# Performance work log

Measured on AMD Instinct MI355X. Metric: run time of the kernel, lower is better.

## Reference

```python
import jax, jax.numpy as jnp
import numpy as np

N, N_EMB, HEAD, N_SEG = 8192, 256, 64, 128  # 128 molecules x 64 atoms


def setup_inputs() -> dict:
    key = jax.random.key(0)
    k0, k1, k2, k3, k4, k5 = jax.random.split(key, 6)
    X = jax.random.normal(k0, (N, N_EMB), dtype=jnp.float32)
    Z = jax.random.normal(k1, (N, 3), dtype=jnp.float32) * 3.0  # coordinates (Angstrom-ish)
    # CSR segment boundaries: 128 equal molecules of 64 atoms
    ptr = jnp.arange(N_SEG + 1, dtype=jnp.int32) * (N // N_SEG)
    scale = 1.0 / np.sqrt(N_EMB)
    Wk = jax.random.normal(k2, (HEAD, N_EMB), dtype=jnp.float32) * scale
    Wq = jax.random.normal(k3, (HEAD, N_EMB), dtype=jnp.float32) * scale
    Wv = jax.random.normal(k4, (HEAD, N_EMB), dtype=jnp.float32) * scale
    # invr0 = (rand(1) + 0.5) / cutoff, cutoff = 4.0
    invr0 = (jax.random.uniform(k5, (1,), dtype=jnp.float32) + 0.5) / 4.0
    return {"X": X, "Z": Z, "Wk": Wk, "Wq": Wq, "Wv": Wv, "invr0": invr0, "ptr": ptr}


def reference(X, Z, Wk, Wq, Wv, invr0, ptr):
    head_size = Wk.shape[0]
    n = X.shape[0]
    K = X @ Wk.T  # [N, H]
    Q = X @ Wq.T  # [N, H]
    V = X @ Wv.T  # [N, H]
    wei = (Q @ K.T) * (head_size ** -0.5)  # [N, N]
    # block-diagonal mask from segment boundaries (== torch.block_diag of ones blocks)
    seg = jnp.searchsorted(ptr[1:], jnp.arange(n, dtype=ptr.dtype), side="right")
    mask = seg[:, None] == seg[None, :]
    wei = jnp.where(mask, wei, -jnp.inf)
    wei = jax.nn.softmax(wei, axis=-1)
    # Euclidean cdist via gram trick, safe sqrt (zero grad at d2<=0, like torch.cdist)
    z2 = jnp.sum(Z * Z, axis=-1)
    d2 = jnp.maximum(z2[:, None] + z2[None, :] - 2.0 * (Z @ Z.T), 0.0)
    dist = jnp.sqrt(jnp.where(d2 > 0, d2, 1.0)) * (d2 > 0)
    wei = wei * jnp.exp(-invr0[0] * dist)
    out = wei @ V  # [N, H]
    return out
```

## Files before the change

### kernel.cpp

```cpp
#include <hip/hip_runtime.h>

#define NATOMS 8192
#define EMB    256
#define HEAD   64
#define LDT    72
#define PB     72

typedef _Float16 f16;
typedef f16   f16x8 __attribute__((ext_vector_type(8)));
typedef f16   f16x4 __attribute__((ext_vector_type(4)));
typedef float f32x4 __attribute__((ext_vector_type(4)));

__global__ __launch_bounds__(512) void fused_kernel(
    const float* __restrict__ X, const float* __restrict__ Z,
    const float* __restrict__ Wk, const float* __restrict__ Wq,
    const float* __restrict__ Wv, const float* __restrict__ invr0p,
    float* __restrict__ out)
{
  union __align__(16) SMem {
    struct {
      f16 Xs[64 * LDT];
      f16 Ws[192 * LDT];
    } a;
    struct {
      f16 Qb[32 * PB];
      f16 Kb[64 * PB];
      f16 Vt[64 * PB];
      f16 Pb[32 * PB];
      float2 part[4][32];
      float zx[64], zy[64], zz[64];
    } b;
  };
  __shared__ SMem sm;

  const int tid  = threadIdx.x;
  const int seg  = blockIdx.x >> 1;
  const int hf   = blockIdx.x & 1;
  const int base = seg * 64;

  const int wave = tid >> 6;
  const int lane = tid & 63;
  const int fr   = lane & 15;
  const int fq   = lane >> 4;
  const int lk   = fq * 8;
  const int mf0  = (wave >> 2) * 2;
  const int nf0  = (wave & 3) * 3;

  f32x4 acc[2][3];
  #pragma unroll
  for (int m = 0; m < 2; ++m)
    #pragma unroll
    for (int n = 0; n < 3; ++n) acc[m][n] = (f32x4){0.f, 0.f, 0.f, 0.f};

  for (int c = 0; c < 4; ++c) {
    const int kc = c * 64;
    #pragma unroll
    for (int i = 0; i < 2; ++i) {
      const int idx = tid + i * 512;
      const int row = idx >> 4;
      const int k4  = (idx & 15) * 4;
      const float4 v = *reinterpret_cast<const float4*>(
          X + (size_t)(base + row) * EMB + kc + k4);
      f16x4 h = {(f16)v.x, (f16)v.y, (f16)v.z, (f16)v.w};
      *reinterpret_cast<f16x4*>(&sm.a.Xs[row * LDT + k4]) = h;
    }
    #pragma unroll
    for (int i = 0; i < 6; ++i) {
      const int idx = tid + i * 512;
      const int wr  = idx >> 4;
      const int k4  = (idx & 15) * 4;
      const float* src = (wr < 64)  ? (Wq + (size_t)wr * EMB)
                       : (wr < 128) ? (Wk + (size_t)(wr - 64) * EMB)
                                    : (Wv + (size_t)(wr - 128) * EMB);
      const float4 v = *reinterpret_cast<const float4*>(src + kc + k4);
      f16x4 h = {(f16)v.x, (f16)v.y, (f16)v.z, (f16)v.w};
      *reinterpret_cast<f16x4*>(&sm.a.Ws[wr * LDT + k4]) = h;
    }
    __syncthreads();

    #pragma unroll
    for (int ks = 0; ks < 2; ++ks) {
      const int hoff = ks * 32 + lk;
      const f16x8 a0 = *reinterpret_cast<const f16x8*>(
          &sm.a.Xs[((mf0 + 0) * 16 + fr) * LDT + hoff]);
      const f16x8 a1 = *reinterpret_cast<const f16x8*>(
          &sm.a.Xs[((mf0 + 1) * 16 + fr) * LDT + hoff]);
      #pragma unroll
      for (int n = 0; n < 3; ++n) {
        const f16x8 b = *reinterpret_cast<const f16x8*>(
            &sm.a.Ws[((nf0 + n) * 16 + fr) * LDT + hoff]);
        acc[0][n] = __builtin_amdgcn_mfma_f32_16x16x32_f16(a0, b, acc[0][n], 0, 0, 0);
        acc[1][n] = __builtin_amdgcn_mfma_f32_16x16x32_f16(a1, b, acc[1][n], 0, 0, 0);
      }
    }
    __syncthreads();
  }

  #pragma unroll
  for (int m = 0; m < 2; ++m) {
    const int mf = mf0 + m;
    const int rr = mf * 16 + fq * 4;
    #pragma unroll
    for (int n = 0; n < 3; ++n) {
      const int nf  = nf0 + n;
      const int col = nf * 16 + fr;
      if (nf < 4) {
        if ((mf >> 1) == hf) {
          const int qr = rr & 31;
          #pragma unroll
          for (int j = 0; j < 4; ++j)
            sm.b.Qb[(qr + j) * PB + col] = (f16)(acc[m][n][j] * 0.125f);
        }
      } else if (nf < 8) {
        #pragma unroll
        for (int j = 0; j < 4; ++j)
          sm.b.Kb[(rr + j) * PB + (col - 64)] = (f16)acc[m][n][j];
      } else {
        f16x4 hv = {(f16)acc[m][n][0], (f16)acc[m][n][1],
                    (f16)acc[m][n][2], (f16)acc[m][n][3]};
        *reinterpret_cast<f16x4*>(&sm.b.Vt[(col - 128) * PB + rr]) = hv;
      }
    }
  }
  if (tid < 64) {
    sm.b.zx[tid] = Z[(size_t)(base + tid) * 3 + 0];
    sm.b.zy[tid] = Z[(size_t)(base + tid) * 3 + 1];
    sm.b.zz[tid] = Z[(size_t)(base + tid) * 3 + 2];
  }
  __syncthreads();

  const int kf = wave & 3;
  const int qf = wave >> 2;
  f32x4 s = (f32x4){0.f, 0.f, 0.f, 0.f};
  #pragma unroll
  for (int hs = 0; hs < 2; ++hs) {
    const int ho = hs * 32 + lk;
    const f16x8 kfrag = *reinterpret_cast<const f16x8*>(
        &sm.b.Kb[(kf * 16 + fr) * PB + ho]);
    const f16x8 qfrag = *reinterpret_cast<const f16x8*>(
        &sm.b.Qb[(qf * 16 + fr) * PB + ho]);
    s = __builtin_amdgcn_mfma_f32_16x16x32_f16(kfrag, qfrag, s, 0, 0, 0);
  }

  float m16 = fmaxf(fmaxf(s[0], s[1]), fmaxf(s[2], s[3]));
  m16 = fmaxf(m16, __shfl_xor(m16, 16));
  m16 = fmaxf(m16, __shfl_xor(m16, 32));
  float e[4]; float s16 = 0.f;
  #pragma unroll
  for (int j = 0; j < 4; ++j) { e[j] = __expf(s[j] - m16); s16 += e[j]; }
  s16 += __shfl_xor(s16, 16);
  s16 += __shfl_xor(s16, 32);
  if (fq == 0) sm.b.part[kf][qf * 16 + fr] = make_float2(m16, s16);
  __syncthreads();

  const float2 p0 = sm.b.part[0][qf * 16 + fr];
  const float2 p1 = sm.b.part[1][qf * 16 + fr];
  const float2 p2 = sm.b.part[2][qf * 16 + fr];
  const float2 p3 = sm.b.part[3][qf * 16 + fr];
  const float mg = fmaxf(fmaxf(p0.x, p1.x), fmaxf(p2.x, p3.x));
  const float sum = p0.y * __expf(p0.x - mg) + p1.y * __expf(p1.x - mg)
                  + p2.y * __expf(p2.x - mg) + p3.y * __expf(p3.x - mg);
  const float myscale = __expf(m16 - mg) / sum;

  const float invr0 = invr0p[0];
  const int   ri = hf * 32 + qf * 16 + fr;
  const float rx = sm.b.zx[ri], ry = sm.b.zy[ri], rz = sm.b.zz[ri];
  f16x4 pv;
  #pragma unroll
  for (int j = 0; j < 4; ++j) {
    const int ka = kf * 16 + fq * 4 + j;
    const float dx = rx - sm.b.zx[ka];
    const float dy = ry - sm.b.zy[ka];
    const float dz = rz - sm.b.zz[ka];
    const float dist = sqrtf(dx * dx + dy * dy + dz * dz);
    pv[j] = (f16)(e[j] * myscale * __expf(-invr0 * dist));
  }
  *reinterpret_cast<f16x4*>(
      &sm.b.Pb[(qf * 16 + fr) * PB + kf * 16 + fq * 4]) = pv;
  __syncthreads();

  const int qf2 = wave & 1;
  const int hb  = wave >> 1;
  f32x4 o = (f32x4){0.f, 0.f, 0.f, 0.f};
  #pragma unroll
  for (int ks2 = 0; ks2 < 2; ++ks2) {
    const int ko = ks2 * 32 + lk;
    const f16x8 pf = *reinterpret_cast<const f16x8*>(
        &sm.b.Pb[(qf2 * 16 + fr) * PB + ko]);
    const f16x8 vf = *reinterpret_cast<const f16x8*>(
        &sm.b.Vt[(hb * 16 + fr) * PB + ko]);
    o = __builtin_amdgcn_mfma_f32_16x16x32_f16(pf, vf, o, 0, 0, 0);
  }
  #pragma unroll
  for (int j = 0; j < 4; ++j)
    out[(size_t)(base + hf * 32 + qf2 * 16 + fq * 4 + j) * HEAD
        + hb * 16 + fr] = o[j];
}

extern "C" void kernel_launch(void* const* d_in, const int* in_sizes, int n_in,
                              void* d_out, int out_size, void* d_ws, size_t ws_size,
                              hipStream_t stream) {
  const float* X     = (const float*)d_in[0];
  const float* Z     = (const float*)d_in[1];
  const float* Wk    = (const float*)d_in[2];
  const float* Wq    = (const float*)d_in[3];
  const float* Wv    = (const float*)d_in[4];
  const float* invr0 = (const float*)d_in[5];

  fused_kernel<<<dim3(NATOMS / 32), dim3(512), 0, stream>>>(
      X, Z, Wk, Wq, Wv, invr0, (float*)d_out);
}
```

Measured before the change: 13.49 us.

## Load full X and W tiles into LDS once instead of four K-chunks

```diff
diff --git a/kernel.cpp b/kernel.cpp
--- a/kernel.cpp
+++ b/kernel.cpp
@@ -3,7 +3,7 @@
 #define NATOMS 8192
 #define EMB    256
 #define HEAD   64
-#define LDT    72
+#define WP     264
 #define PB     72
 
 typedef _Float16 f16;
@@ -19,8 +19,8 @@
 {
   union __align__(16) SMem {
     struct {
-      f16 Xs[64 * LDT];
-      f16 Ws[192 * LDT];
+      f16 Xs[64 * WP];
+      f16 Ws[192 * WP];
     } a;
     struct {
       f16 Qb[32 * PB];
@@ -42,9 +42,64 @@
   const int lane = tid & 63;
   const int fr   = lane & 15;
   const int fq   = lane >> 4;
-  const int lk   = fq * 8;
   const int mf0  = (wave >> 2) * 2;
   const int nf0  = (wave & 3) * 3;
+
+  const float ir = invr0p[0];
+  float zr0 = 0.f, zr1 = 0.f, zr2 = 0.f;
+  if (tid < 64) {
+    const float* zp = Z + (size_t)(base + tid) * 3;
+    zr0 = zp[0]; zr1 = zp[1]; zr2 = zp[2];
+  }
+
+  float4 xv[8];
+  #pragma unroll
+  for (int i = 0; i < 8; ++i) {
+    const int f = tid + i * 512;
+    const int row = f >> 6, c4 = f & 63;
+    xv[i] = *reinterpret_cast<const float4*>(
+        X + (size_t)(base + row) * EMB + c4 * 4);
+  }
+  float4 wv1[12];
+  #pragma unroll
+  for (int i = 0; i < 12; ++i) {
+    const int f = tid + i * 512;
+    const int row = f >> 6, c4 = f & 63;
+    const float* src = (row < 64) ? (Wq + (size_t)row * EMB)
+                                  : (Wk + (size_t)(row - 64) * EMB);
+    wv1[i] = *reinterpret_cast<const float4*>(src + c4 * 4);
+  }
+  #pragma unroll
+  for (int i = 0; i < 8; ++i) {
+    const int f = tid + i * 512;
+    const int row = f >> 6, c4 = f & 63;
+    f16x4 h = {(f16)xv[i].x, (f16)xv[i].y, (f16)xv[i].z, (f16)xv[i].w};
+    *reinterpret_cast<f16x4*>(&sm.a.Xs[row * WP + c4 * 4]) = h;
+  }
+  float4 wv2[12];
+  #pragma unroll
+  for (int i = 0; i < 12; ++i) {
+    const int f = tid + (12 + i) * 512;
+    const int row = f >> 6, c4 = f & 63;
+    const float* src = (row < 128) ? (Wk + (size_t)(row - 64) * EMB)
+                                   : (Wv + (size_t)(row - 128) * EMB);
+    wv2[i] = *reinterpret_cast<const float4*>(src + c4 * 4);
+  }
+  #pragma unroll
+  for (int i = 0; i < 12; ++i) {
+    const int f = tid + i * 512;
+    const int row = f >> 6, c4 = f & 63;
+    f16x4 h = {(f16)wv1[i].x, (f16)wv1[i].y, (f16)wv1[i].z, (f16)wv1[i].w};
+    *reinterpret_cast<f16x4*>(&sm.a.Ws[row * WP + c4 * 4]) = h;
+  }
+  #pragma unroll
+  for (int i = 0; i < 12; ++i) {
+    const int f = tid + (12 + i) * 512;
+    const int row = f >> 6, c4 = f & 63;
+    f16x4 h = {(f16)wv2[i].x, (f16)wv2[i].y, (f16)wv2[i].z, (f16)wv2[i].w};
+    *reinterpret_cast<f16x4*>(&sm.a.Ws[row * WP + c4 * 4]) = h;
+  }
+  __syncthreads();
 
   f32x4 acc[2][3];
   #pragma unroll
@@ -52,49 +107,25 @@
     #pragma unroll
     for (int n = 0; n < 3; ++n) acc[m][n] = (f32x4){0.f, 0.f, 0.f, 0.f};
 
+  #pragma unroll
   for (int c = 0; c < 4; ++c) {
-    const int kc = c * 64;
-    #pragma unroll
-    for (int i = 0; i < 2; ++i) {
-      const int idx = tid + i * 512;
-      const int row = idx >> 4;
-      const int k4  = (idx & 15) * 4;
-      const float4 v = *reinterpret_cast<const float4*>(
-          X + (size_t)(base + row) * EMB + kc + k4);
-      f16x4 h = {(f16)v.x, (f16)v.y, (f16)v.z, (f16)v.w};
-      *reinterpret_cast<f16x4*>(&sm.a.Xs[row * LDT + k4]) = h;
-    }
-    #pragma unroll
-    for (int i = 0; i < 6; ++i) {
-      const int idx = tid + i * 512;
-      const int wr  = idx >> 4;
-      const int k4  = (idx & 15) * 4;
-      const float* src = (wr < 64)  ? (Wq + (size_t)wr * EMB)
-                       : (wr < 128) ? (Wk + (size_t)(wr - 64) * EMB)
-                                    : (Wv + (size_t)(wr - 128) * EMB);
-      const float4 v = *reinterpret_cast<const float4*>(src + kc + k4);
-      f16x4 h = {(f16)v.x, (f16)v.y, (f16)v.z, (f16)v.w};
-      *reinterpret_cast<f16x4*>(&sm.a.Ws[wr * LDT + k4]) = h;
-    }
-    __syncthreads();
-
     #pragma unroll
     for (int ks = 0; ks < 2; ++ks) {
-      const int hoff = ks * 32 + lk;
+      const int ko = c * 64 + ks * 32 + fq * 8;
       const f16x8 a0 = *reinterpret_cast<const f16x8*>(
-          &sm.a.Xs[((mf0 + 0) * 16 + fr) * LDT + hoff]);
+          &sm.a.Xs[((mf0 + 0) * 16 + fr) * WP + ko]);
       const f16x8 a1 = *reinterpret_cast<const f16x8*>(
-          &sm.a.Xs[((mf0 + 1) * 16 + fr) * LDT + hoff]);
+          &sm.a.Xs[((mf0 + 1) * 16 + fr) * WP + ko]);
       #pragma unroll
       for (int n = 0; n < 3; ++n) {
         const f16x8 b = *reinterpret_cast<const f16x8*>(
-            &sm.a.Ws[((nf0 + n) * 16 + fr) * LDT + hoff]);
+            &sm.a.Ws[((nf0 + n) * 16 + fr) * WP + ko]);
         acc[0][n] = __builtin_amdgcn_mfma_f32_16x16x32_f16(a0, b, acc[0][n], 0, 0, 0);
         acc[1][n] = __builtin_amdgcn_mfma_f32_16x16x32_f16(a1, b, acc[1][n], 0, 0, 0);
       }
     }
-    __syncthreads();
-  }
+  }
+  __syncthreads();
 
   #pragma unroll
   for (int m = 0; m < 2; ++m) {
@@ -123,9 +154,7 @@
     }
   }
   if (tid < 64) {
-    sm.b.zx[tid] = Z[(size_t)(base + tid) * 3 + 0];
-    sm.b.zy[tid] = Z[(size_t)(base + tid) * 3 + 1];
-    sm.b.zz[tid] = Z[(size_t)(base + tid) * 3 + 2];
+    sm.b.zx[tid] = zr0; sm.b.zy[tid] = zr1; sm.b.zz[tid] = zr2;
   }
   __syncthreads();
 
@@ -134,7 +163,7 @@
   f32x4 s = (f32x4){0.f, 0.f, 0.f, 0.f};
   #pragma unroll
   for (int hs = 0; hs < 2; ++hs) {
-    const int ho = hs * 32 + lk;
+    const int ho = hs * 32 + fq * 8;
     const f16x8 kfrag = *reinterpret_cast<const f16x8*>(
         &sm.b.Kb[(kf * 16 + fr) * PB + ho]);
     const f16x8 qfrag = *reinterpret_cast<const f16x8*>(
@@ -162,7 +191,6 @@
                   + p2.y * __expf(p2.x - mg) + p3.y * __expf(p3.x - mg);
   const float myscale = __expf(m16 - mg) / sum;
 
-  const float invr0 = invr0p[0];
   const int   ri = hf * 32 + qf * 16 + fr;
   const float rx = sm.b.zx[ri], ry = sm.b.zy[ri], rz = sm.b.zz[ri];
   f16x4 pv;
@@ -173,7 +201,7 @@
     const float dy = ry - sm.b.zy[ka];
     const float dz = rz - sm.b.zz[ka];
     const float dist = sqrtf(dx * dx + dy * dy + dz * dz);
-    pv[j] = (f16)(e[j] * myscale * __expf(-invr0 * dist));
+    pv[j] = (f16)(e[j] * myscale * __expf(-ir * dist));
   }
   *reinterpret_cast<f16x4*>(
       &sm.b.Pb[(qf * 16 + fr) * PB + kf * 16 + fq * 4]) = pv;
@@ -184,11 +212,11 @@
   f32x4 o = (f32x4){0.f, 0.f, 0.f, 0.f};
   #pragma unroll
   for (int ks2 = 0; ks2 < 2; ++ks2) {
-    const int ko = ks2 * 32 + lk;
+    const int ko2 = ks2 * 32 + fq * 8;
     const f16x8 pf = *reinterpret_cast<const f16x8*>(
-        &sm.b.Pb[(qf2 * 16 + fr) * PB + ko]);
+        &sm.b.Pb[(qf2 * 16 + fr) * PB + ko2]);
     const f16x8 vf = *reinterpret_cast<const f16x8*>(
-        &sm.b.Vt[(hb * 16 + fr) * PB + ko]);
+        &sm.b.Vt[(hb * 16 + fr) * PB + ko2]);
     o = __builtin_amdgcn_mfma_f32_16x16x32_f16(pf, vf, o, 0, 0, 0);
   }
   #pragma unroll
```

After: 12.05 us (median of 2 runs). 1.12x faster.
